# Performance work log

Measured on AMD Instinct MI355X. Metric: run time of the kernel, lower is better.

Reference implementation:

```python
import jax, jax.numpy as jnp
import numpy as np

S, B, H = 1024, 4096, 8  # seq_len, batch, hidden (=input) size


def setup_inputs() -> dict:
    key = jax.random.key(0)
    k0, k1, k2, k3, k4 = jax.random.split(key, 5)
    scale = 1.0 / np.sqrt(H)  # matches torch uniform(-1/sqrt(H), 1/sqrt(H)) magnitude
    return {
        "input_": jax.random.normal(k0, (S, B, H), dtype=jnp.float32),
        "w_ih": jax.random.uniform(k1, (3 * H, H), jnp.float32, -scale, scale),
        "w_hh": jax.random.uniform(k2, (3 * H, H), jnp.float32, -scale, scale),
        "b_ih": jax.random.uniform(k3, (3 * H,), jnp.float32, -scale, scale),
        "b_hh": jax.random.uniform(k4, (3 * H,), jnp.float32, -scale, scale),
    }


def _gru_seq(input_, w_ih, w_hh, b_ih, b_hh):
    # Precompute input-side gate projections for all timesteps in one GEMM:
    # (S, B, 3H); gate order in PyTorch GRU is r, z, n.
    xg = jnp.einsum("sbi,gi->sbg", input_, w_ih) + b_ih
    h0 = jnp.zeros((input_.shape[1], w_hh.shape[1]), dtype=input_.dtype)

    def step(h, xg_t):
        hg = h @ w_hh.T + b_hh                      # (B, 3H)
        xr, xz, xn = jnp.split(xg_t, 3, axis=-1)
        hr, hz, hn = jnp.split(hg, 3, axis=-1)
        r = jax.nn.sigmoid(xr + hr)
        z = jax.nn.sigmoid(xz + hz)
        n = jnp.tanh(xn + r * hn)
        h_new = (1.0 - z) * n + z * h
        return h_new, h_new

    h_last, outputs = jax.lax.scan(step, h0, xg)
    return outputs, h_last[None]  # (S, B, H), (1, B, H) like torch GRU


def reference(input_, w_ih, w_hh, b_ih, b_hh):
    return _gru_seq(input_, w_ih, w_hh, b_ih, b_hh)
```

## Files before the change

kernel.cpp:

```cpp
#include <hip/hip_runtime.h>

#define SS 1024
#define BB 4096
#define HH 8
#define XSTRIDE (BB * HH)

typedef float f32x2 __attribute__((ext_vector_type(2)));

__device__ __forceinline__ int dpp_x1(int v) {
    return __builtin_amdgcn_mov_dpp(v, 0xB1, 0xF, 0xF, true);
}
__device__ __forceinline__ int dpp_x2(int v) {
    return __builtin_amdgcn_mov_dpp(v, 0x4E, 0xF, 0xF, true);
}
__device__ __forceinline__ int dpp_x7(int v) {
    return __builtin_amdgcn_mov_dpp(v, 0x141, 0xF, 0xF, true);
}

__device__ __constant__ int MK_[8] = {0, 1, 2, 3, 7, 6, 5, 4};

#define ALOAD(DST, PTR) asm volatile("global_load_dwordx4 %0, %1, off" : "=v"(DST) : "v"(PTR))

#define LOADG(BUF, GRP) do {                                                           \
    const float* bp_ = xp + (size_t)(GRP) * 8 * XSTRIDE;                               \
    _Pragma("unroll")                                                                  \
    for (int u_ = 0; u_ < 8; ++u_) {                                                   \
        const float* p_ = bp_ + (size_t)u_ * XSTRIDE;                                  \
        ALOAD(BUF[2 * u_],     p_);                                                    \
        ALOAD(BUF[2 * u_ + 1], p_ + 4);                                                \
    }                                                                                  \
} while (0)

#define WAITV(N) do {                                                                  \
    asm volatile("s_waitcnt vmcnt(" #N ")" ::: "memory");                              \
    __builtin_amdgcn_sched_barrier(0);                                                 \
} while (0)

#define XFULL(BUF, V) do {                                                             \
    const float4 Xa_ = BUF[2 * (V)], Xb_ = BUF[2 * (V) + 1];                           \
    f32x2 a0_ = {Xa_.x, Xa_.y}, a1_ = {Xa_.z, Xa_.w};                                  \
    f32x2 a2_ = {Xb_.x, Xb_.y}, a3_ = {Xb_.z, Xb_.w};                                  \
    f32x2 sr_ = {bias_r, 0.0f}, sz_ = {bias_z, 0.0f}, sn_ = {bni_s, 0.0f};             \
    sr_ = __builtin_elementwise_fma(a0_, wri[0], sr_);                                 \
    sz_ = __builtin_elementwise_fma(a0_, wzi[0], sz_);                                 \
    sn_ = __builtin_elementwise_fma(a0_, wni[0], sn_);                                 \
    sr_ = __builtin_elementwise_fma(a1_, wri[1], sr_);                                 \
    sz_ = __builtin_elementwise_fma(a1_, wzi[1], sz_);                                 \
    sn_ = __builtin_elementwise_fma(a1_, wni[1], sn_);                                 \
    sr_ = __builtin_elementwise_fma(a2_, wri[2], sr_);                                 \
    sz_ = __builtin_elementwise_fma(a2_, wzi[2], sz_);                                 \
    sn_ = __builtin_elementwise_fma(a2_, wni[2], sn_);                                 \
    sr_ = __builtin_elementwise_fma(a3_, wri[3], sr_);                                 \
    sz_ = __builtin_elementwise_fma(a3_, wzi[3], sz_);                                 \
    sn_ = __builtin_elementwise_fma(a3_, wni[3], sn_);                                 \
    xr[(V)] = sr_.x + sr_.y; xz[(V)] = sz_.x + sz_.y; xn[(V)] = sn_.x + sn_.y;         \
} while (0)

#define GROUP(BUF, SBASE) do {                                                         \
    XFULL(BUF, 0);                                                                     \
    XFULL(BUF, 1);                                                                     \
    _Pragma("unroll")                                                                  \
    for (int u = 0; u < 8; ++u) {                                                      \
        f32x2 hr2 = {xr[u], 0.0f}, hz2 = {xz[u], 0.0f}, hn2 = {bnh_s, 0.0f};           \
        _Pragma("unroll")                                                              \
        for (int p_ = 0; p_ < 4; ++p_) {                                               \
            hr2 = __builtin_elementwise_fma(hv2[p_], wrh[p_], hr2);                    \
            hz2 = __builtin_elementwise_fma(hv2[p_], wzh[p_], hz2);                    \
            hn2 = __builtin_elementwise_fma(hv2[p_], wnh[p_], hn2);                    \
        }                                                                              \
        const float srr = hr2.x + hr2.y;                                               \
        const float szz = hz2.x + hz2.y;                                               \
        const float snn = hn2.x + hn2.y;                                               \
        const bool W = (u + 2 < 8);                                                    \
        f32x2 sr_, sz_, sn_;                                                           \
        if (W) {                   \
            const float4 Xa_ = BUF[2 * (u + 2)];                                       \
            f32x2 a0_ = {Xa_.x, Xa_.y}, a1_ = {Xa_.z, Xa_.w};                          \
            sr_ = (f32x2){bias_r, 0.0f}; sz_ = (f32x2){bias_z, 0.0f};                  \
            sn_ = (f32x2){bni_s, 0.0f};                                                \
            sr_ = __builtin_elementwise_fma(a0_, wri[0], sr_);                         \
            sz_ = __builtin_elementwise_fma(a0_, wzi[0], sz_);                         \
            sn_ = __builtin_elementwise_fma(a0_, wni[0], sn_);                         \
            sr_ = __builtin_elementwise_fma(a1_, wri[1], sr_);                         \
            sz_ = __builtin_elementwise_fma(a1_, wzi[1], sz_);                         \
            sn_ = __builtin_elementwise_fma(a1_, wni[1], sn_);                         \
        }                                                                              \
        const float er = __builtin_amdgcn_exp2f(srr);                                  \
        const float ez = __builtin_amdgcn_exp2f(szz);                                  \
        if (W) {                     \
            const float4 Xb_ = BUF[2 * (u + 2) + 1];                                   \
            f32x2 a2_ = {Xb_.x, Xb_.y}, a3_ = {Xb_.z, Xb_.w};                          \
            sr_ = __builtin_elementwise_fma(a2_, wri[2], sr_);                         \
            sz_ = __builtin_elementwise_fma(a2_, wzi[2], sz_);                         \
            sn_ = __builtin_elementwise_fma(a2_, wni[2], sn_);                         \
            sr_ = __builtin_elementwise_fma(a3_, wri[3], sr_);                         \
            sz_ = __builtin_elementwise_fma(a3_, wzi[3], sz_);                         \
            sn_ = __builtin_elementwise_fma(a3_, wni[3], sn_);                         \
        }                                                                              \
        const float r_ = __builtin_amdgcn_rcpf(1.0f + er);                             \
        const float z_ = __builtin_amdgcn_rcpf(1.0f + ez);                             \
        if (W) {                                \
            xr[u + 2] = sr_.x + sr_.y;                                                 \
            xz[u + 2] = sz_.x + sz_.y;                                                 \
            xn[u + 2] = sn_.x + sn_.y;                                                 \
        }                                                                              \
        const float en = __builtin_amdgcn_exp2f(fmaf(r_, snn, xn[u]));                 \
        const float n_ = fmaf(-2.0f, __builtin_amdgcn_rcpf(1.0f + en), 1.0f);          \
        h = n_ + z_ * (h - n_);                                                        \
        const int hb_ = __float_as_int(h);                                             \
        const int t1_ = dpp_x1(hb_);                                                   \
        const int t2_ = dpp_x2(hb_);                                                   \
        const int t3_ = dpp_x2(t1_);                                                   \
        const int t4_ = dpp_x7(hb_);                                                   \
        const int t5_ = dpp_x7(t1_);                                                   \
        const int t6_ = dpp_x7(t2_);                                                   \
        const int t7_ = dpp_x7(t3_);                                                   \
        hv2[0] = (f32x2){h, __int_as_float(t1_)};                                      \
        hv2[1] = (f32x2){__int_as_float(t2_), __int_as_float(t3_)};                    \
        hv2[2] = (f32x2){__int_as_float(t4_), __int_as_float(t5_)};                    \
        hv2[3] = (f32x2){__int_as_float(t6_), __int_as_float(t7_)};                    \
        __builtin_nontemporal_store(h, &op[(size_t)((SBASE) + u) * XSTRIDE]);          \
    }                                                                                  \
} while (0)

__global__ __launch_bounds__(64, 1) void gru_kernel(
    const float* __restrict__ x,
    const float* __restrict__ w_ih,
    const float* __restrict__ w_hh,
    const float* __restrict__ b_ih,
    const float* __restrict__ b_hh,
    float* __restrict__ out)
{
    const int lane = threadIdx.x;
    const int j = lane & 7;
    const int bg = (blockIdx.x << 3) + (lane >> 3);

    const float SR = -1.4426950408889634f;
    const float SN = 2.8853900817779268f;

    f32x2 wri[4], wzi[4], wni[4];
    #pragma unroll
    for (int p = 0; p < 4; ++p) {
        wri[p] = (f32x2){SR * w_ih[j * 8 + 2 * p],        SR * w_ih[j * 8 + 2 * p + 1]};
        wzi[p] = (f32x2){SR * w_ih[(8 + j) * 8 + 2 * p],  SR * w_ih[(8 + j) * 8 + 2 * p + 1]};
        wni[p] = (f32x2){SN * w_ih[(16 + j) * 8 + 2 * p], SN * w_ih[(16 + j) * 8 + 2 * p + 1]};
    }
    f32x2 wrh[4], wzh[4], wnh[4];
    #pragma unroll
    for (int p = 0; p < 4; ++p) {
        const int c0 = j ^ MK_[2 * p], c1 = j ^ MK_[2 * p + 1];
        wrh[p] = (f32x2){SR * w_hh[j * 8 + c0],        SR * w_hh[j * 8 + c1]};
        wzh[p] = (f32x2){SR * w_hh[(8 + j) * 8 + c0],  SR * w_hh[(8 + j) * 8 + c1]};
        wnh[p] = (f32x2){SN * w_hh[(16 + j) * 8 + c0], SN * w_hh[(16 + j) * 8 + c1]};
    }
    const float bias_r = SR * (b_ih[j] + b_hh[j]);
    const float bias_z = SR * (b_ih[8 + j] + b_hh[8 + j]);
    const float bni_s  = SN * b_ih[16 + j];
    const float bnh_s  = SN * b_hh[16 + j];

    const float* xp = x + (size_t)bg * HH;
    float* op = out + (size_t)bg * HH + j;
    float* hlast = out + (size_t)SS * BB * HH + (size_t)bg * HH + j;

    float4 xA[16], xB[16];

    LOADG(xA, 0);
    LOADG(xB, 1);
    WAITV(16);

    float h = 0.0f;
    f32x2 hv2[4] = {{0,0},{0,0},{0,0},{0,0}};
    float xr[8], xz[8], xn[8];

    for (int g = 0; g < 128; g += 2) {
        GROUP(xA, g * 8);
        {
            const int ga = (g + 2 < 128) ? (g + 2) : 127;
            LOADG(xA, ga);
        }
        WAITV(24);
        GROUP(xB, (g + 1) * 8);
        {
            const int gb = (g + 3 < 128) ? (g + 3) : 127;
            LOADG(xB, gb);
        }
        WAITV(24);
    }
    *hlast = h;
}

extern "C" void kernel_launch(void* const* d_in, const int* in_sizes, int n_in,
                              void* d_out, int out_size, void* d_ws, size_t ws_size,
                              hipStream_t stream) {
    const float* x    = (const float*)d_in[0];
    const float* w_ih = (const float*)d_in[1];
    const float* w_hh = (const float*)d_in[2];
    const float* b_ih = (const float*)d_in[3];
    const float* b_hh = (const float*)d_in[4];
    float* out = (float*)d_out;
    gru_kernel<<<BB / 8, 64, 0, stream>>>(x, w_ih, w_hh, b_ih, b_hh, out);
}
```

Baseline: 134.8 us.

## Interleave next-group loads into recurrence tail and split FMA chains

Prefetch loads for the next group are now issued inside the last two timesteps of each group, once their buffer slots are free, instead of as a burst after the group. They use an SGPR base plus per-lane VGPR byte offsets. The hidden-state matvec is split into two independent accumulators to shorten the serial FMA chain on the recurrence critical path. One DPP chain is replaced by a direct swizzle, and the final groups are peeled so the redundant clamped reloads are skipped. The risk is that the extra VGPRs for the offsets, or a changed schedule, add stalls within each step.

Result: slower. 147.7 us (+9.6%).

```diff
diff --git a/kernel.cpp b/kernel.cpp
--- a/kernel.cpp
+++ b/kernel.cpp
@@ -4,32 +4,19 @@
 #define BB 4096
 #define HH 8
 #define XSTRIDE (BB * HH)
+#define GBYTES (8 * XSTRIDE * 4)
 
 typedef float f32x2 __attribute__((ext_vector_type(2)));
 
-__device__ __forceinline__ int dpp_x1(int v) {
-    return __builtin_amdgcn_mov_dpp(v, 0xB1, 0xF, 0xF, true);
-}
-__device__ __forceinline__ int dpp_x2(int v) {
-    return __builtin_amdgcn_mov_dpp(v, 0x4E, 0xF, 0xF, true);
-}
-__device__ __forceinline__ int dpp_x7(int v) {
-    return __builtin_amdgcn_mov_dpp(v, 0x141, 0xF, 0xF, true);
-}
+__device__ __forceinline__ int dpp_x1(int v) { return __builtin_amdgcn_mov_dpp(v, 0xB1, 0xF, 0xF, true); }
+__device__ __forceinline__ int dpp_x2(int v) { return __builtin_amdgcn_mov_dpp(v, 0x4E, 0xF, 0xF, true); }
+__device__ __forceinline__ int dpp_x3(int v) { return __builtin_amdgcn_mov_dpp(v, 0x1B, 0xF, 0xF, true); }
+__device__ __forceinline__ int dpp_x7(int v) { return __builtin_amdgcn_mov_dpp(v, 0x141, 0xF, 0xF, true); }
 
 __device__ __constant__ int MK_[8] = {0, 1, 2, 3, 7, 6, 5, 4};
 
-#define ALOAD(DST, PTR) asm volatile("global_load_dwordx4 %0, %1, off" : "=v"(DST) : "v"(PTR))
-
-#define LOADG(BUF, GRP) do {                                                           \
-    const float* bp_ = xp + (size_t)(GRP) * 8 * XSTRIDE;                               \
-    _Pragma("unroll")                                                                  \
-    for (int u_ = 0; u_ < 8; ++u_) {                                                   \
-        const float* p_ = bp_ + (size_t)u_ * XSTRIDE;                                  \
-        ALOAD(BUF[2 * u_],     p_);                                                    \
-        ALOAD(BUF[2 * u_ + 1], p_ + 4);                                                \
-    }                                                                                  \
-} while (0)
+#define ALOADS(DST, OFF) \
+    asm volatile("global_load_dwordx4 %0, %1, %2" : "=v"(DST) : "v"(OFF), "s"(x))
 
 #define WAITV(N) do {                                                                  \
     asm volatile("s_waitcnt vmcnt(" #N ")" ::: "memory");                              \
@@ -56,24 +43,34 @@
     xr[(V)] = sr_.x + sr_.y; xz[(V)] = sz_.x + sz_.y; xn[(V)] = sn_.x + sn_.y;         \
 } while (0)
 
-#define GROUP(BUF, SBASE) do {                                                         \
+#define GROUP(BUF, SBASE, DL) do {                                                     \
     XFULL(BUF, 0);                                                                     \
     XFULL(BUF, 1);                                                                     \
     _Pragma("unroll")                                                                  \
     for (int u = 0; u < 8; ++u) {                                                      \
-        f32x2 hr2 = {xr[u], 0.0f}, hz2 = {xz[u], 0.0f}, hn2 = {bnh_s, 0.0f};           \
-        _Pragma("unroll")                                                              \
-        for (int p_ = 0; p_ < 4; ++p_) {                                               \
-            hr2 = __builtin_elementwise_fma(hv2[p_], wrh[p_], hr2);                    \
-            hz2 = __builtin_elementwise_fma(hv2[p_], wzh[p_], hz2);                    \
-            hn2 = __builtin_elementwise_fma(hv2[p_], wnh[p_], hn2);                    \
-        }                                                                              \
-        const float srr = hr2.x + hr2.y;                                               \
-        const float szz = hz2.x + hz2.y;                                               \
-        const float snn = hn2.x + hn2.y;                                               \
+        const int k0 = (u >= 6) ? (u - 6) * 8 : 0;                                     \
+                  \
+        f32x2 rA = {xr[u], 0.0f}, zA = {xz[u], 0.0f}, nA = {bnh_s, 0.0f};              \
+        f32x2 rB = {0.0f, 0.0f}, zB = {0.0f, 0.0f}, nB = {0.0f, 0.0f};                 \
+        rA = __builtin_elementwise_fma(hv2[0], wrh[0], rA);                            \
+        zA = __builtin_elementwise_fma(hv2[0], wzh[0], zA);                            \
+        nA = __builtin_elementwise_fma(hv2[0], wnh[0], nA);                            \
+        rB = __builtin_elementwise_fma(hv2[2], wrh[2], rB);                            \
+        zB = __builtin_elementwise_fma(hv2[2], wzh[2], zB);                            \
+        nB = __builtin_elementwise_fma(hv2[2], wnh[2], nB);                            \
+        rA = __builtin_elementwise_fma(hv2[1], wrh[1], rA);                            \
+        zA = __builtin_elementwise_fma(hv2[1], wzh[1], zA);                            \
+        nA = __builtin_elementwise_fma(hv2[1], wnh[1], nA);                            \
+        rB = __builtin_elementwise_fma(hv2[3], wrh[3], rB);                            \
+        zB = __builtin_elementwise_fma(hv2[3], wzh[3], zB);                            \
+        nB = __builtin_elementwise_fma(hv2[3], wnh[3], nB);                            \
+        rA = rA + rB; zA = zA + zB; nA = nA + nB;                                      \
+        const float srr = rA.x + rA.y;                                                 \
+        const float szz = zA.x + zA.y;                                                 \
+        const float snn = nA.x + nA.y;                                                 \
         const bool W = (u + 2 < 8);                                                    \
         f32x2 sr_, sz_, sn_;                                                           \
-        if (W) {                   \
+        if (W) {                                                    \
             const float4 Xa_ = BUF[2 * (u + 2)];                                       \
             f32x2 a0_ = {Xa_.x, Xa_.y}, a1_ = {Xa_.z, Xa_.w};                          \
             sr_ = (f32x2){bias_r, 0.0f}; sz_ = (f32x2){bias_z, 0.0f};                  \
@@ -84,10 +81,14 @@
             sr_ = __builtin_elementwise_fma(a1_, wri[1], sr_);                         \
             sz_ = __builtin_elementwise_fma(a1_, wzi[1], sz_);                         \
             sn_ = __builtin_elementwise_fma(a1_, wni[1], sn_);                         \
+        } else if (DL) {                                                               \
+            ALOADS(BUF[k0 + 0], off[k0 + 0]);                                          \
+            ALOADS(BUF[k0 + 1], off[k0 + 1]);                                          \
+            ALOADS(BUF[k0 + 2], off[k0 + 2]);                                          \
         }                                                                              \
         const float er = __builtin_amdgcn_exp2f(srr);                                  \
         const float ez = __builtin_amdgcn_exp2f(szz);                                  \
-        if (W) {                     \
+        if (W) {                                                    \
             const float4 Xb_ = BUF[2 * (u + 2) + 1];                                   \
             f32x2 a2_ = {Xb_.x, Xb_.y}, a3_ = {Xb_.z, Xb_.w};                          \
             sr_ = __builtin_elementwise_fma(a2_, wri[2], sr_);                         \
@@ -96,34 +97,53 @@
             sr_ = __builtin_elementwise_fma(a3_, wri[3], sr_);                         \
             sz_ = __builtin_elementwise_fma(a3_, wzi[3], sz_);                         \
             sn_ = __builtin_elementwise_fma(a3_, wni[3], sn_);                         \
+        } else if (DL) {                                                               \
+            ALOADS(BUF[k0 + 3], off[k0 + 3]);                                          \
+            ALOADS(BUF[k0 + 4], off[k0 + 4]);                                          \
+            ALOADS(BUF[k0 + 5], off[k0 + 5]);                                          \
         }                                                                              \
         const float r_ = __builtin_amdgcn_rcpf(1.0f + er);                             \
         const float z_ = __builtin_amdgcn_rcpf(1.0f + ez);                             \
-        if (W) {                                \
+        if (W) {                                                    \
             xr[u + 2] = sr_.x + sr_.y;                                                 \
             xz[u + 2] = sz_.x + sz_.y;                                                 \
             xn[u + 2] = sn_.x + sn_.y;                                                 \
+        } else if (DL) {                                                               \
+            ALOADS(BUF[k0 + 6], off[k0 + 6]);                                          \
+            ALOADS(BUF[k0 + 7], off[k0 + 7]);                                          \
         }                                                                              \
         const float en = __builtin_amdgcn_exp2f(fmaf(r_, snn, xn[u]));                 \
         const float n_ = fmaf(-2.0f, __builtin_amdgcn_rcpf(1.0f + en), 1.0f);          \
         h = n_ + z_ * (h - n_);                                                        \
         const int hb_ = __float_as_int(h);                                             \
-        const int t1_ = dpp_x1(hb_);                                                   \
-        const int t2_ = dpp_x2(hb_);                                                   \
-        const int t3_ = dpp_x2(t1_);                                                   \
-        const int t4_ = dpp_x7(hb_);                                                   \
-        const int t5_ = dpp_x7(t1_);                                                   \
-        const int t6_ = dpp_x7(t2_);                                                   \
-        const int t7_ = dpp_x7(t3_);                                                   \
+        const int t1_ = dpp_x1(hb_);                                       \
+        const int t2_ = dpp_x2(hb_);                                       \
+        const int t3_ = dpp_x3(hb_);                     \
+        const int t4_ = dpp_x7(hb_);                                       \
+        const int t5_ = dpp_x7(t1_);                                       \
+        const int t6_ = dpp_x7(t2_);                                       \
+        const int t7_ = dpp_x7(t3_);                             \
         hv2[0] = (f32x2){h, __int_as_float(t1_)};                                      \
         hv2[1] = (f32x2){__int_as_float(t2_), __int_as_float(t3_)};                    \
         hv2[2] = (f32x2){__int_as_float(t4_), __int_as_float(t5_)};                    \
         hv2[3] = (f32x2){__int_as_float(t6_), __int_as_float(t7_)};                    \
         __builtin_nontemporal_store(h, &op[(size_t)((SBASE) + u) * XSTRIDE]);          \
     }                                                                                  \
-} while (0)
-
-__global__ __launch_bounds__(64, 1) void gru_kernel(
+    if (DL) {                                                                          \
+        _Pragma("unroll")                                                              \
+        for (int k_ = 0; k_ < 16; ++k_) off[k_] += GBYTES;                             \
+    }                                                                                  \
+} while (0)
+
+#define LOADGP(BUF) do {                                                               \
+    _Pragma("unroll")                                                                  \
+    for (int k_ = 0; k_ < 16; ++k_) ALOADS(BUF[k_], off[k_]);                          \
+    _Pragma("unroll")                                                                  \
+    for (int k_ = 0; k_ < 16; ++k_) off[k_] += GBYTES;                                 \
+} while (0)
+
+__global__ __launch_bounds__(64) __attribute__((amdgpu_waves_per_eu(1, 1)))
+void gru_kernel(
     const float* __restrict__ x,
     const float* __restrict__ w_ih,
     const float* __restrict__ w_hh,
@@ -158,34 +178,38 @@
     const float bni_s  = SN * b_ih[16 + j];
     const float bnh_s  = SN * b_hh[16 + j];
 
-    const float* xp = x + (size_t)bg * HH;
     float* op = out + (size_t)bg * HH + j;
     float* hlast = out + (size_t)SS * BB * HH + (size_t)bg * HH + j;
 
+    int off[16];
+    #pragma unroll
+    for (int k = 0; k < 16; ++k)
+        off[k] = bg * (HH * 4) + (k >> 1) * (XSTRIDE * 4) + (k & 1) * 16;
+
     float4 xA[16], xB[16];
 
-    LOADG(xA, 0);
-    LOADG(xB, 1);
+    LOADGP(xA);
+    LOADGP(xB);
     WAITV(16);
 
     float h = 0.0f;
     f32x2 hv2[4] = {{0,0},{0,0},{0,0},{0,0}};
     float xr[8], xz[8], xn[8];
 
-    for (int g = 0; g < 128; g += 2) {
-        GROUP(xA, g * 8);
-        {
-            const int ga = (g + 2 < 128) ? (g + 2) : 127;
-            LOADG(xA, ga);
-        }
+    for (int g = 0; g < 124; g += 2) {
+        GROUP(xA, g * 8, 1);
         WAITV(24);
-        GROUP(xB, (g + 1) * 8);
-        {
-            const int gb = (g + 3 < 128) ? (g + 3) : 127;
-            LOADG(xB, gb);
-        }
+        GROUP(xB, (g + 1) * 8, 1);
         WAITV(24);
     }
+    GROUP(xA, 124 * 8, 1);
+    WAITV(24);
+    GROUP(xB, 125 * 8, 1);
+    WAITV(24);
+    GROUP(xA, 126 * 8, 0);
+    WAITV(8);
+    GROUP(xB, 127 * 8, 0);
+
     *hlast = h;
 }
 
```

## Load one x element per lane and broadcast across the group via DPP

Applied to the files above, without the earlier changes.

Each lane now issues one dword load per timestep instead of two dwordx4 loads of the full 8-wide input row. The row is rebuilt in registers with the same DPP butterfly already used to share h. The w_ih columns are permuted to match that order. This cuts redundant global load traffic and vector registers, but adds DPP moves on the input projection path. The tail of the loop is peeled so that out-of-range reloads and the clamped index are gone.

After: 144.9 us. 1.08x slower.

```diff
diff --git a/kernel.cpp b/kernel.cpp
--- a/kernel.cpp
+++ b/kernel.cpp
@@ -7,52 +7,44 @@
 
 typedef float f32x2 __attribute__((ext_vector_type(2)));
 
-__device__ __forceinline__ int dpp_x1(int v) {
-    return __builtin_amdgcn_mov_dpp(v, 0xB1, 0xF, 0xF, true);
-}
-__device__ __forceinline__ int dpp_x2(int v) {
-    return __builtin_amdgcn_mov_dpp(v, 0x4E, 0xF, 0xF, true);
-}
-__device__ __forceinline__ int dpp_x7(int v) {
-    return __builtin_amdgcn_mov_dpp(v, 0x141, 0xF, 0xF, true);
-}
+__device__ __forceinline__ int dpp_x1(int v) { return __builtin_amdgcn_mov_dpp(v, 0xB1, 0xF, 0xF, true); }
+__device__ __forceinline__ int dpp_x2(int v) { return __builtin_amdgcn_mov_dpp(v, 0x4E, 0xF, 0xF, true); }
+__device__ __forceinline__ int dpp_x7(int v) { return __builtin_amdgcn_mov_dpp(v, 0x141, 0xF, 0xF, true); }
 
 __device__ __constant__ int MK_[8] = {0, 1, 2, 3, 7, 6, 5, 4};
 
-#define ALOAD(DST, PTR) asm volatile("global_load_dwordx4 %0, %1, off" : "=v"(DST) : "v"(PTR))
-
-#define LOADG(BUF, GRP) do {                                                           \
-    const float* bp_ = xp + (size_t)(GRP) * 8 * XSTRIDE;                               \
-    _Pragma("unroll")                                                                  \
-    for (int u_ = 0; u_ < 8; ++u_) {                                                   \
-        const float* p_ = bp_ + (size_t)u_ * XSTRIDE;                                  \
-        ALOAD(BUF[2 * u_],     p_);                                                    \
-        ALOAD(BUF[2 * u_ + 1], p_ + 4);                                                \
-    }                                                                                  \
-} while (0)
+#define ALOADD(DST, PTR) asm volatile("global_load_dword %0, %1, off" : "=v"(DST) : "v"(PTR))
 
 #define WAITV(N) do {                                                                  \
     asm volatile("s_waitcnt vmcnt(" #N ")" ::: "memory");                              \
     __builtin_amdgcn_sched_barrier(0);                                                 \
 } while (0)
 
+#define BFLY8(SRC, DV) do {                                                            \
+    const int b0_ = __float_as_int(SRC);                                               \
+    const int b1_ = dpp_x1(b0_);                                                       \
+    const int b2_ = dpp_x2(b0_);                                                       \
+    const int b3_ = dpp_x2(b1_);                                                       \
+    const int b4_ = dpp_x7(b0_);                                                       \
+    const int b5_ = dpp_x7(b1_);                                                       \
+    const int b6_ = dpp_x7(b2_);                                                       \
+    const int b7_ = dpp_x7(b3_);                                                       \
+    DV[0] = (f32x2){(SRC), __int_as_float(b1_)};                                       \
+    DV[1] = (f32x2){__int_as_float(b2_), __int_as_float(b3_)};                         \
+    DV[2] = (f32x2){__int_as_float(b4_), __int_as_float(b5_)};                         \
+    DV[3] = (f32x2){__int_as_float(b6_), __int_as_float(b7_)};                         \
+} while (0)
+
 #define XFULL(BUF, V) do {                                                             \
-    const float4 Xa_ = BUF[2 * (V)], Xb_ = BUF[2 * (V) + 1];                           \
-    f32x2 a0_ = {Xa_.x, Xa_.y}, a1_ = {Xa_.z, Xa_.w};                                  \
-    f32x2 a2_ = {Xb_.x, Xb_.y}, a3_ = {Xb_.z, Xb_.w};                                  \
+    f32x2 xv_[4];                                                                      \
+    BFLY8(BUF[V], xv_);                                                                \
     f32x2 sr_ = {bias_r, 0.0f}, sz_ = {bias_z, 0.0f}, sn_ = {bni_s, 0.0f};             \
-    sr_ = __builtin_elementwise_fma(a0_, wri[0], sr_);                                 \
-    sz_ = __builtin_elementwise_fma(a0_, wzi[0], sz_);                                 \
-    sn_ = __builtin_elementwise_fma(a0_, wni[0], sn_);                                 \
-    sr_ = __builtin_elementwise_fma(a1_, wri[1], sr_);                                 \
-    sz_ = __builtin_elementwise_fma(a1_, wzi[1], sz_);                                 \
-    sn_ = __builtin_elementwise_fma(a1_, wni[1], sn_);                                 \
-    sr_ = __builtin_elementwise_fma(a2_, wri[2], sr_);                                 \
-    sz_ = __builtin_elementwise_fma(a2_, wzi[2], sz_);                                 \
-    sn_ = __builtin_elementwise_fma(a2_, wni[2], sn_);                                 \
-    sr_ = __builtin_elementwise_fma(a3_, wri[3], sr_);                                 \
-    sz_ = __builtin_elementwise_fma(a3_, wzi[3], sz_);                                 \
-    sn_ = __builtin_elementwise_fma(a3_, wni[3], sn_);                                 \
+    _Pragma("unroll")                                                                  \
+    for (int p_ = 0; p_ < 4; ++p_) {                                                   \
+        sr_ = __builtin_elementwise_fma(xv_[p_], wri[p_], sr_);                        \
+        sz_ = __builtin_elementwise_fma(xv_[p_], wzi[p_], sz_);                        \
+        sn_ = __builtin_elementwise_fma(xv_[p_], wni[p_], sn_);                        \
+    }                                                                                  \
     xr[(V)] = sr_.x + sr_.y; xz[(V)] = sz_.x + sz_.y; xn[(V)] = sn_.x + sn_.y;         \
 } while (0)
 
@@ -61,6 +53,7 @@
     XFULL(BUF, 1);                                                                     \
     _Pragma("unroll")                                                                  \
     for (int u = 0; u < 8; ++u) {                                                      \
+                                \
         f32x2 hr2 = {xr[u], 0.0f}, hz2 = {xz[u], 0.0f}, hn2 = {bnh_s, 0.0f};           \
         _Pragma("unroll")                                                              \
         for (int p_ = 0; p_ < 4; ++p_) {                                               \
@@ -72,34 +65,31 @@
         const float szz = hz2.x + hz2.y;                                               \
         const float snn = hn2.x + hn2.y;                                               \
         const bool W = (u + 2 < 8);                                                    \
-        f32x2 sr_, sz_, sn_;                                                           \
-        if (W) {                   \
-            const float4 Xa_ = BUF[2 * (u + 2)];                                       \
-            f32x2 a0_ = {Xa_.x, Xa_.y}, a1_ = {Xa_.z, Xa_.w};                          \
+        f32x2 xv_[4], sr_, sz_, sn_;                                                   \
+        if (W) {                        \
+            BFLY8(BUF[u + 2], xv_);                                                    \
             sr_ = (f32x2){bias_r, 0.0f}; sz_ = (f32x2){bias_z, 0.0f};                  \
             sn_ = (f32x2){bni_s, 0.0f};                                                \
-            sr_ = __builtin_elementwise_fma(a0_, wri[0], sr_);                         \
-            sz_ = __builtin_elementwise_fma(a0_, wzi[0], sz_);                         \
-            sn_ = __builtin_elementwise_fma(a0_, wni[0], sn_);                         \
-            sr_ = __builtin_elementwise_fma(a1_, wri[1], sr_);                         \
-            sz_ = __builtin_elementwise_fma(a1_, wzi[1], sz_);                         \
-            sn_ = __builtin_elementwise_fma(a1_, wni[1], sn_);                         \
+            sr_ = __builtin_elementwise_fma(xv_[0], wri[0], sr_);                      \
+            sz_ = __builtin_elementwise_fma(xv_[0], wzi[0], sz_);                      \
+            sn_ = __builtin_elementwise_fma(xv_[0], wni[0], sn_);                      \
+            sr_ = __builtin_elementwise_fma(xv_[1], wri[1], sr_);                      \
+            sz_ = __builtin_elementwise_fma(xv_[1], wzi[1], sz_);                      \
+            sn_ = __builtin_elementwise_fma(xv_[1], wni[1], sn_);                      \
         }                                                                              \
         const float er = __builtin_amdgcn_exp2f(srr);                                  \
         const float ez = __builtin_amdgcn_exp2f(szz);                                  \
-        if (W) {                     \
-            const float4 Xb_ = BUF[2 * (u + 2) + 1];                                   \
-            f32x2 a2_ = {Xb_.x, Xb_.y}, a3_ = {Xb_.z, Xb_.w};                          \
-            sr_ = __builtin_elementwise_fma(a2_, wri[2], sr_);                         \
-            sz_ = __builtin_elementwise_fma(a2_, wzi[2], sz_);                         \
-            sn_ = __builtin_elementwise_fma(a2_, wni[2], sn_);                         \
-            sr_ = __builtin_elementwise_fma(a3_, wri[3], sr_);                         \
-            sz_ = __builtin_elementwise_fma(a3_, wzi[3], sz_);                         \
-            sn_ = __builtin_elementwise_fma(a3_, wni[3], sn_);                         \
+        if (W) {                                     \
+            sr_ = __builtin_elementwise_fma(xv_[2], wri[2], sr_);                      \
+            sz_ = __builtin_elementwise_fma(xv_[2], wzi[2], sz_);                      \
+            sn_ = __builtin_elementwise_fma(xv_[2], wni[2], sn_);                      \
+            sr_ = __builtin_elementwise_fma(xv_[3], wri[3], sr_);                      \
+            sz_ = __builtin_elementwise_fma(xv_[3], wzi[3], sz_);                      \
+            sn_ = __builtin_elementwise_fma(xv_[3], wni[3], sn_);                      \
         }                                                                              \
         const float r_ = __builtin_amdgcn_rcpf(1.0f + er);                             \
         const float z_ = __builtin_amdgcn_rcpf(1.0f + ez);                             \
-        if (W) {                                \
+        if (W) {                                                    \
             xr[u + 2] = sr_.x + sr_.y;                                                 \
             xz[u + 2] = sz_.x + sz_.y;                                                 \
             xn[u + 2] = sn_.x + sn_.y;                                                 \
@@ -123,6 +113,12 @@
     }                                                                                  \
 } while (0)
 
+#define LOADG(BUF, GRP) do {                                                           \
+    const float* bp_ = xq + (size_t)(GRP) * 8 * XSTRIDE;                               \
+    _Pragma("unroll")                                                                  \
+    for (int u_ = 0; u_ < 8; ++u_) ALOADD(BUF[u_], bp_ + (size_t)u_ * XSTRIDE);        \
+} while (0)
+
 __global__ __launch_bounds__(64, 1) void gru_kernel(
     const float* __restrict__ x,
     const float* __restrict__ w_ih,
@@ -133,22 +129,17 @@
 {
     const int lane = threadIdx.x;
     const int j = lane & 7;
-    const int bg = (blockIdx.x << 3) + (lane >> 3);
 
     const float SR = -1.4426950408889634f;
     const float SN = 2.8853900817779268f;
 
-    f32x2 wri[4], wzi[4], wni[4];
-    #pragma unroll
-    for (int p = 0; p < 4; ++p) {
-        wri[p] = (f32x2){SR * w_ih[j * 8 + 2 * p],        SR * w_ih[j * 8 + 2 * p + 1]};
-        wzi[p] = (f32x2){SR * w_ih[(8 + j) * 8 + 2 * p],  SR * w_ih[(8 + j) * 8 + 2 * p + 1]};
-        wni[p] = (f32x2){SN * w_ih[(16 + j) * 8 + 2 * p], SN * w_ih[(16 + j) * 8 + 2 * p + 1]};
-    }
-    f32x2 wrh[4], wzh[4], wnh[4];
+    f32x2 wri[4], wzi[4], wni[4], wrh[4], wzh[4], wnh[4];
     #pragma unroll
     for (int p = 0; p < 4; ++p) {
         const int c0 = j ^ MK_[2 * p], c1 = j ^ MK_[2 * p + 1];
+        wri[p] = (f32x2){SR * w_ih[j * 8 + c0],        SR * w_ih[j * 8 + c1]};
+        wzi[p] = (f32x2){SR * w_ih[(8 + j) * 8 + c0],  SR * w_ih[(8 + j) * 8 + c1]};
+        wni[p] = (f32x2){SN * w_ih[(16 + j) * 8 + c0], SN * w_ih[(16 + j) * 8 + c1]};
         wrh[p] = (f32x2){SR * w_hh[j * 8 + c0],        SR * w_hh[j * 8 + c1]};
         wzh[p] = (f32x2){SR * w_hh[(8 + j) * 8 + c0],  SR * w_hh[(8 + j) * 8 + c1]};
         wnh[p] = (f32x2){SN * w_hh[(16 + j) * 8 + c0], SN * w_hh[(16 + j) * 8 + c1]};
@@ -158,34 +149,33 @@
     const float bni_s  = SN * b_ih[16 + j];
     const float bnh_s  = SN * b_hh[16 + j];
 
-    const float* xp = x + (size_t)bg * HH;
-    float* op = out + (size_t)bg * HH + j;
-    float* hlast = out + (size_t)SS * BB * HH + (size_t)bg * HH + j;
+    const float* xq = x + (blockIdx.x << 6) + lane;
+    float* op = out + (blockIdx.x << 6) + lane;
+    float* hlast = out + (size_t)SS * BB * HH + (blockIdx.x << 6) + lane;
 
-    float4 xA[16], xB[16];
+    float xA[8], xB[8];
 
     LOADG(xA, 0);
     LOADG(xB, 1);
-    WAITV(16);
+    WAITV(8);
 
     float h = 0.0f;
     f32x2 hv2[4] = {{0,0},{0,0},{0,0},{0,0}};
     float xr[8], xz[8], xn[8];
 
-    for (int g = 0; g < 128; g += 2) {
+    for (int g = 0; g < 124; g += 2) {
         GROUP(xA, g * 8);
-        {
-            const int ga = (g + 2 < 128) ? (g + 2) : 127;
-            LOADG(xA, ga);
-        }
-        WAITV(24);
+        LOADG(xA, g + 2);
+        WAITV(16);
         GROUP(xB, (g + 1) * 8);
-        {
-            const int gb = (g + 3 < 128) ? (g + 3) : 127;
-            LOADG(xB, gb);
-        }
-        WAITV(24);
+        LOADG(xB, g + 3);
+        WAITV(16);
     }
+    GROUP(xA, 992);  LOADG(xA, 126); WAITV(16);
+    GROUP(xB, 1000); LOADG(xB, 127); WAITV(16);
+    GROUP(xA, 1008); WAITV(8);
+    GROUP(xB, 1016);
+
     *hlast = h;
 }
 
```
